# Kernel tuning notes

Hardware: AMD Instinct MI355X
Metric: run time of the kernel (lower is better)

The kernel has to match this reference:

```python
import jax, jax.numpy as jnp
import numpy as np

N, D = 8192, 128
EPS = 1e-6  # torch F.pairwise_distance default eps


def _pe(d, s=3, t=2):
    # 1/d^s - 1/d^t
    return 1.0 / (d ** s) - 1.0 / (d ** t)


def setup_inputs() -> dict:
    key = jax.random.key(0)
    x = jax.random.normal(key, (N, D), dtype=jnp.float32)
    return {"x": x}


def reference(x):
    n = x.shape[0]
    # loss0: distance of each row to the origin; torch pairwise_distance adds eps to the diff
    d0 = jnp.sqrt(jnp.sum((x + EPS) ** 2, axis=-1))  # [N]
    loss0 = jnp.mean(jnp.clip(_pe(d0), -1.5, 1000.0))

    # pdist: condensed upper-triangular pairwise Euclidean distances (no eps)
    sq = jnp.sum(x * x, axis=-1)                      # [N]
    d2 = sq[:, None] + sq[None, :] - 2.0 * (x @ x.T)  # [N, N]
    mask = jnp.triu(jnp.ones((n, n), dtype=bool), k=1)
    # keep masked entries at 1.0 so sqrt/pe stay finite
    d2 = jnp.where(mask, jnp.maximum(d2, 0.0), 1.0)
    d = jnp.sqrt(d2)
    vals = jnp.clip(_pe(d), -1.5, 1000.0)
    cnt = n * (n - 1) // 2
    loss = jnp.sum(jnp.where(mask, vals, 0.0)) / cnt
    return loss0 + loss
```

## Files before the change

kernel.cpp:

```cpp
#include <hip/hip_runtime.h>
#include <hip/hip_bf16.h>


#define NROWS 8192
#define DDIM  128
#define TILE  128
#define RB    128
#define TTILES (NROWS / TILE)
#define NTRI  (TTILES * (TTILES + 1) / 2)
#define NBLKP 1024
#define FEPS  1e-6f

typedef float f32x4 __attribute__((ext_vector_type(4)));
typedef long long i64;

__global__ __launch_bounds__(256) void convert_kernel(
        const float* __restrict__ x, unsigned short* __restrict__ xf8_u16,
        float* __restrict__ sq, float* __restrict__ p0) {
    int tid = threadIdx.x;
    int wave = tid >> 6, lane = tid & 63;
    int row = blockIdx.x * 4 + wave;

    float2 v = *(const float2*)(x + (size_t)row * DDIM + lane * 2);
    float s = v.x * v.x + v.y * v.y;
    float ex = v.x + FEPS, ey = v.y + FEPS;
    float e = ex * ex + ey * ey;

    int packed = __builtin_amdgcn_cvt_pk_fp8_f32(v.x, v.y, 0, false);
    xf8_u16[(size_t)row * 64 + lane] = (unsigned short)(packed & 0xFFFF);

    #pragma unroll
    for (int off = 32; off; off >>= 1) {
        s += __shfl_down(s, off);
        e += __shfl_down(e, off);
    }

    __shared__ float red[4];
    if (lane == 0) {
        sq[row] = s;
        float r = rsqrtf(e);
        float r2 = r * r;
        red[wave] = fminf(fmaxf(r2 * r - r2, -1.5f), 1000.0f);
    }
    __syncthreads();
    if (tid == 0) p0[blockIdx.x] = red[0] + red[1] + red[2] + red[3];
}

__device__ __forceinline__ int tri_off(int i) {
    return i * TTILES - ((i * (i - 1)) >> 1);
}

__device__ __forceinline__ void stage_tile(const char* __restrict__ g,
                                           char* lds, int tid) {
    uint4 v[2];
    #pragma unroll
    for (int p = 0; p < 2; ++p)
        v[p] = *(const uint4*)(g + (p * 512 + tid) * 16);
    #pragma unroll
    for (int p = 0; p < 2; ++p) {
        int n = p * 512 + tid;
        int row = n >> 3, c = n & 7;
        *(uint4*)(lds + row * RB + ((c * 16) ^ ((row & 7) << 4))) = v[p];
    }
}

__global__ __launch_bounds__(512, 4) void pair_kernel(
        const unsigned short* __restrict__ xf8_u16,
        const float* __restrict__ sq, float* __restrict__ pp) {
    const char* xb = (const char*)xf8_u16;
    __shared__ char smem[32768];
    char* ldsA = smem;
    char* ldsB = smem + 16384;

    int b = blockIdx.x;
    int t0, cnt;
    if (b < 32) { t0 = b * 3; cnt = 3; }
    else        { t0 = 96 + (b - 32) * 2; cnt = 2; }

    int I = 0;
    {
        float T2 = 2.0f * TTILES + 1.0f;
        I = (int)((T2 - sqrtf(T2 * T2 - 8.0f * (float)t0)) * 0.5f);
        while (tri_off(I + 1) <= t0) ++I;
        while (tri_off(I) > t0) --I;
    }
    int J = I + (t0 - tri_off(I));

    int tid = threadIdx.x;
    int wave = tid >> 6, lane = tid & 63;
    int wR = (wave >> 2) * 64;
    int wC = (wave & 3) * 32;
    int lcol = lane & 15;
    int lrow = lane >> 4;

    float lsum = 0.0f;
    int curI = -1;

    for (int k = 0; k < cnt; ++k) {
        if (I != curI) { stage_tile(xb + (size_t)I * TILE * RB, ldsA, tid); curI = I; }
        bool diag = (I == J);
        if (!diag) stage_tile(xb + (size_t)J * TILE * RB, ldsB, tid);
        __syncthreads();
        const char* bufB = diag ? ldsA : ldsB;

        f32x4 acc[4][2];
        #pragma unroll
        for (int r = 0; r < 4; ++r)
            #pragma unroll
            for (int c = 0; c < 2; ++c) acc[r][c] = (f32x4){0.f, 0.f, 0.f, 0.f};

        #pragma unroll
        for (int ks = 0; ks < 4; ++ks) {
            int koff = ks * 32 + lrow * 8;
            i64 a[4], bb[2];
            #pragma unroll
            for (int r = 0; r < 4; ++r) {
                int row = wR + r * 16 + lcol;
                a[r] = *(const i64*)(ldsA + row * RB + (koff ^ ((row & 7) << 4)));
            }
            #pragma unroll
            for (int c = 0; c < 2; ++c) {
                int row = wC + c * 16 + lcol;
                bb[c] = *(const i64*)(bufB + row * RB + (koff ^ ((row & 7) << 4)));
            }
            #pragma unroll
            for (int r = 0; r < 4; ++r)
                #pragma unroll
                for (int c = 0; c < 2; ++c)
                    acc[r][c] = __builtin_amdgcn_mfma_f32_16x16x32_fp8_fp8(
                        a[r], bb[c], acc[r][c], 0, 0, 0);
        }

        int ibase = I * TILE + wR + lrow * 4;
        int jbase = J * TILE + wC + lcol;
        float sqj[2];
        #pragma unroll
        for (int c = 0; c < 2; ++c) sqj[c] = sq[jbase + c * 16];

        if (!diag) {
            #pragma unroll
            for (int r = 0; r < 4; ++r)
                #pragma unroll
                for (int u = 0; u < 4; ++u) {
                    float si = sq[ibase + r * 16 + u];
                    #pragma unroll
                    for (int c = 0; c < 2; ++c) {
                        float d2 = si + sqj[c] - 2.0f * acc[r][c][u];
                        float rv = rsqrtf(d2);
                        float r2 = rv * rv;
                        lsum += r2 * rv - r2;
                    }
                }
        } else {
            int il0 = wR + lrow * 4;
            int jl0 = wC + lcol;
            #pragma unroll
            for (int r = 0; r < 4; ++r)
                #pragma unroll
                for (int u = 0; u < 4; ++u) {
                    int il = il0 + r * 16 + u;
                    float si = sq[ibase + r * 16 + u];
                    #pragma unroll
                    for (int c = 0; c < 2; ++c) {
                        if (jl0 + c * 16 > il) {
                            float d2 = fmaxf(si + sqj[c] - 2.0f * acc[r][c][u], 1e-30f);
                            float rv = rsqrtf(d2);
                            float r2 = rv * rv;
                            lsum += fminf(r2 * rv - r2, 1000.0f);
                        }
                    }
                }
        }
        __syncthreads();

        ++J;
        if (J == TTILES) { ++I; J = I; }
    }

    #pragma unroll
    for (int off = 32; off; off >>= 1) lsum += __shfl_down(lsum, off);
    __shared__ float red[8];
    if (lane == 0) red[wave] = lsum;
    __syncthreads();
    if (tid == 0) {
        float t = 0.f;
        #pragma unroll
        for (int w = 0; w < 8; ++w) t += red[w];
        pp[blockIdx.x] = t;
    }
}

__global__ __launch_bounds__(1024) void reduce_kernel(
        const float* __restrict__ p0, int n0,
        const float* __restrict__ pp, int np, float* __restrict__ out) {
    int tid = threadIdx.x;
    double s0 = 0.0, sp = 0.0;
    for (int i = tid; i < n0; i += 1024) s0 += (double)p0[i];
    for (int i = tid; i < np; i += 1024) sp += (double)pp[i];
    __shared__ double sh0[1024], shp[1024];
    sh0[tid] = s0; shp[tid] = sp;
    __syncthreads();
    for (int s = 512; s; s >>= 1) {
        if (tid < s) { sh0[tid] += sh0[tid + s]; shp[tid] += shp[tid + s]; }
        __syncthreads();
    }
    if (tid == 0) {
        double cnt = (double)NROWS * (double)(NROWS - 1) * 0.5;
        out[0] = (float)(sh0[0] / (double)NROWS + shp[0] / cnt);
    }
}

extern "C" void kernel_launch(void* const* d_in, const int* in_sizes, int n_in,
                              void* d_out, int out_size, void* d_ws, size_t ws_size,
                              hipStream_t stream) {
    const float* x = (const float*)d_in[0];
    char* ws = (char*)d_ws;
    const size_t OFF_SQ = 1048576;
    const size_t OFF_P0 = OFF_SQ + 32768;
    const size_t OFF_PP = OFF_P0 + 8192;
    if (ws_size < OFF_PP + NBLKP * sizeof(float)) return;

    unsigned short* xf8 = (unsigned short*)ws;
    float* sq = (float*)(ws + OFF_SQ);
    float* p0 = (float*)(ws + OFF_P0);
    float* pp = (float*)(ws + OFF_PP);

    convert_kernel<<<NROWS / 4, 256, 0, stream>>>(x, xf8, sq, p0);
    pair_kernel<<<NBLKP, 512, 0, stream>>>(xf8, sq, pp);
    reduce_kernel<<<1, 1024, 0, stream>>>(p0, NROWS / 4, pp, NBLKP, (float*)d_out);
}
```

Baseline: 33.27 us.

## Assign each block up to four same-row tiles and stage two B tiles per barrier

Work is redistributed so each block owns one row tile I and up to four consecutive column tiles, which lets the A tile and its row norms be loaded once per block. B tiles are staged two at a time into a doubled LDS buffer, halving the number of barrier pairs per tile. The grid shrinks from 1024 to 544 blocks, and LDS per block grows to 48 KB, which may limit occupancy. Load balance also becomes uneven because row tiles near the end have fewer column tiles.

```diff
diff --git a/kernel.cpp b/kernel.cpp
--- a/kernel.cpp
+++ b/kernel.cpp
@@ -7,8 +7,7 @@
 #define TILE  128
 #define RB    128
 #define TTILES (NROWS / TILE)
-#define NTRI  (TTILES * (TTILES + 1) / 2)
-#define NBLKP 1024
+#define NBLKP 544
 #define FEPS  1e-6f
 
 typedef float f32x4 __attribute__((ext_vector_type(4)));
@@ -46,10 +45,6 @@
     if (tid == 0) p0[blockIdx.x] = red[0] + red[1] + red[2] + red[3];
 }
 
-__device__ __forceinline__ int tri_off(int i) {
-    return i * TTILES - ((i * (i - 1)) >> 1);
-}
-
 __device__ __forceinline__ void stage_tile(const char* __restrict__ g,
                                            char* lds, int tid) {
     uint4 v[2];
@@ -68,23 +63,15 @@
         const unsigned short* __restrict__ xf8_u16,
         const float* __restrict__ sq, float* __restrict__ pp) {
     const char* xb = (const char*)xf8_u16;
-    __shared__ char smem[32768];
+    __shared__ char smem[49152];
     char* ldsA = smem;
-    char* ldsB = smem + 16384;
-
-    int b = blockIdx.x;
-    int t0, cnt;
-    if (b < 32) { t0 = b * 3; cnt = 3; }
-    else        { t0 = 96 + (b - 32) * 2; cnt = 2; }
-
-    int I = 0;
-    {
-        float T2 = 2.0f * TTILES + 1.0f;
-        I = (int)((T2 - sqrtf(T2 * T2 - 8.0f * (float)t0)) * 0.5f);
-        while (tri_off(I + 1) <= t0) ++I;
-        while (tri_off(I) > t0) --I;
-    }
-    int J = I + (t0 - tri_off(I));
+    char* ldsB[2] = { smem + 16384, smem + 32768 };
+
+    int s = blockIdx.x, I = 0;
+    int ns = (TTILES + 3) / 4;
+    while (s >= ns) { s -= ns; ++I; ns = (TTILES - I + 3) / 4; }
+    int j0 = I + s * 4;
+    int jend = j0 + 4; if (jend > TTILES) jend = TTILES;
 
     int tid = threadIdx.x;
     int wave = tid >> 6, lane = tid & 63;
@@ -93,88 +80,103 @@
     int lcol = lane & 15;
     int lrow = lane >> 4;
 
+    stage_tile(xb + (size_t)I * TILE * RB, ldsA, tid);
+    int ibase = I * TILE + wR + lrow * 4;
+    float sqi[4][4];
+    #pragma unroll
+    for (int r = 0; r < 4; ++r)
+        #pragma unroll
+        for (int u = 0; u < 4; ++u) sqi[r][u] = sq[ibase + r * 16 + u];
+    int il0 = wR + lrow * 4;
+    int jl0 = wC + lcol;
+
     float lsum = 0.0f;
-    int curI = -1;
-
-    for (int k = 0; k < cnt; ++k) {
-        if (I != curI) { stage_tile(xb + (size_t)I * TILE * RB, ldsA, tid); curI = I; }
-        bool diag = (I == J);
-        if (!diag) stage_tile(xb + (size_t)J * TILE * RB, ldsB, tid);
+
+    int J = j0;
+    while (J < jend) {
+        int n = (jend - J >= 2) ? 2 : 1;
+
+        #pragma unroll
+        for (int q = 0; q < 2; ++q)
+            if (q < n && J + q != I)
+                stage_tile(xb + (size_t)(J + q) * TILE * RB, ldsB[q], tid);
         __syncthreads();
-        const char* bufB = diag ? ldsA : ldsB;
-
-        f32x4 acc[4][2];
-        #pragma unroll
-        for (int r = 0; r < 4; ++r)
-            #pragma unroll
-            for (int c = 0; c < 2; ++c) acc[r][c] = (f32x4){0.f, 0.f, 0.f, 0.f};
-
-        #pragma unroll
-        for (int ks = 0; ks < 4; ++ks) {
-            int koff = ks * 32 + lrow * 8;
-            i64 a[4], bb[2];
-            #pragma unroll
-            for (int r = 0; r < 4; ++r) {
-                int row = wR + r * 16 + lcol;
-                a[r] = *(const i64*)(ldsA + row * RB + (koff ^ ((row & 7) << 4)));
-            }
-            #pragma unroll
-            for (int c = 0; c < 2; ++c) {
-                int row = wC + c * 16 + lcol;
-                bb[c] = *(const i64*)(bufB + row * RB + (koff ^ ((row & 7) << 4)));
-            }
+
+        #pragma unroll
+        for (int q = 0; q < 2; ++q) {
+            if (q >= n) break;
+            int Jq = J + q;
+            bool diag = (Jq == I);
+            const char* bufB = diag ? ldsA : ldsB[q];
+
+            f32x4 acc[4][2];
             #pragma unroll
             for (int r = 0; r < 4; ++r)
                 #pragma unroll
-                for (int c = 0; c < 2; ++c)
-                    acc[r][c] = __builtin_amdgcn_mfma_f32_16x16x32_fp8_fp8(
-                        a[r], bb[c], acc[r][c], 0, 0, 0);
-        }
-
-        int ibase = I * TILE + wR + lrow * 4;
-        int jbase = J * TILE + wC + lcol;
-        float sqj[2];
-        #pragma unroll
-        for (int c = 0; c < 2; ++c) sqj[c] = sq[jbase + c * 16];
-
-        if (!diag) {
+                for (int c = 0; c < 2; ++c) acc[r][c] = (f32x4){0.f, 0.f, 0.f, 0.f};
+
             #pragma unroll
-            for (int r = 0; r < 4; ++r)
-                #pragma unroll
-                for (int u = 0; u < 4; ++u) {
-                    float si = sq[ibase + r * 16 + u];
+            for (int ks = 0; ks < 4; ++ks) {
+                int koff = ks * 32 + lrow * 8;
+                i64 a[4], bb[2];
+                #pragma unroll
+                for (int r = 0; r < 4; ++r) {
+                    int row = wR + r * 16 + lcol;
+                    a[r] = *(const i64*)(ldsA + row * RB + (koff ^ ((row & 7) << 4)));
+                }
+                #pragma unroll
+                for (int c = 0; c < 2; ++c) {
+                    int row = wC + c * 16 + lcol;
+                    bb[c] = *(const i64*)(bufB + row * RB + (koff ^ ((row & 7) << 4)));
+                }
+                #pragma unroll
+                for (int r = 0; r < 4; ++r)
                     #pragma unroll
-                    for (int c = 0; c < 2; ++c) {
-                        float d2 = si + sqj[c] - 2.0f * acc[r][c][u];
-                        float rv = rsqrtf(d2);
-                        float r2 = rv * rv;
-                        lsum += r2 * rv - r2;
-                    }
-                }
-        } else {
-            int il0 = wR + lrow * 4;
-            int jl0 = wC + lcol;
+                    for (int c = 0; c < 2; ++c)
+                        acc[r][c] = __builtin_amdgcn_mfma_f32_16x16x32_fp8_fp8(
+                            a[r], bb[c], acc[r][c], 0, 0, 0);
+            }
+
+            int jbase = Jq * TILE + wC + lcol;
+            float sqj[2];
             #pragma unroll
-            for (int r = 0; r < 4; ++r)
-                #pragma unroll
-                for (int u = 0; u < 4; ++u) {
-                    int il = il0 + r * 16 + u;
-                    float si = sq[ibase + r * 16 + u];
+            for (int c = 0; c < 2; ++c) sqj[c] = sq[jbase + c * 16];
+
+            if (!diag) {
+                #pragma unroll
+                for (int r = 0; r < 4; ++r)
                     #pragma unroll
-                    for (int c = 0; c < 2; ++c) {
-                        if (jl0 + c * 16 > il) {
-                            float d2 = fmaxf(si + sqj[c] - 2.0f * acc[r][c][u], 1e-30f);
+                    for (int u = 0; u < 4; ++u) {
+                        float si = sqi[r][u];
+                        #pragma unroll
+                        for (int c = 0; c < 2; ++c) {
+                            float d2 = si + sqj[c] - 2.0f * acc[r][c][u];
                             float rv = rsqrtf(d2);
                             float r2 = rv * rv;
-                            lsum += fminf(r2 * rv - r2, 1000.0f);
+                            lsum += r2 * rv - r2;
                         }
                     }
-                }
+            } else {
+                #pragma unroll
+                for (int r = 0; r < 4; ++r)
+                    #pragma unroll
+                    for (int u = 0; u < 4; ++u) {
+                        int il = il0 + r * 16 + u;
+                        float si = sqi[r][u];
+                        #pragma unroll
+                        for (int c = 0; c < 2; ++c) {
+                            if (jl0 + c * 16 > il) {
+                                float d2 = fmaxf(si + sqj[c] - 2.0f * acc[r][c][u], 1e-30f);
+                                float rv = rsqrtf(d2);
+                                float r2 = rv * rv;
+                                lsum += fminf(r2 * rv - r2, 1000.0f);
+                            }
+                        }
+                    }
+            }
         }
         __syncthreads();
-
-        ++J;
-        if (J == TTILES) { ++I; J = I; }
+        J += n;
     }
 
     #pragma unroll
```

Result: slower. 36.17 us (+8.7%).
